# Kernel optimization log

Hardware: AMD Instinct MI355X
Metric: run time of the kernel (lower is better)

Reference implementation:

```python
import jax, jax.numpy as jnp
import numpy as np

B, N, D = 8192, 8192, 768

def setup_inputs() -> dict:
    key = jax.random.key(0)
    kx, ky = jax.random.split(key)
    x = jax.random.normal(kx, (B, D), dtype=jnp.float32)
    y = jax.random.normal(ky, (N, D), dtype=jnp.float32)
    return {"x": x, "y": y}

def reference(x, y):
    # Pairwise squared L2 distances: ||x_i - y_j||^2 = ||x_i||^2 + ||y_j||^2 - 2 x_i . y_j
    # Mathematically identical to the naive broadcast (x[:,None,:]-y[None,:,:])**2 sum,
    # but avoids the O(B*N*D) intermediate. Clamp at 0 to guard fp cancellation
    # (true squared distances are nonnegative).
    x2 = jnp.sum(x * x, axis=-1)[:, None]           # [B, 1]
    y2 = jnp.sum(y * y, axis=-1)[None, :]           # [1, N]
    xy = jnp.einsum('bd,nd->bn', x, y)              # [B, N] GEMM
    d = x2 + y2 - 2.0 * xy
    return jnp.maximum(d, 0.0)
```

## Files before the change

kernel.cpp:

```cpp
#include <hip/hip_runtime.h>
#include <hip/hip_bf16.h>
#include <stdint.h>


#define M_DIM 8192
#define N_DIM 8192
#define D_DIM 768
#define K_DIM (3 * D_DIM)
#define BM 256
#define BN 256
#define BK 32
#define KT (K_DIM / BK)

typedef __bf16 bf16x8 __attribute__((ext_vector_type(8)));
typedef float f32x4 __attribute__((ext_vector_type(4)));

#define GLOAD_LDS16(g, l) \
  __builtin_amdgcn_global_load_lds((const __attribute__((address_space(1))) void*)(g), \
                                   (__attribute__((address_space(3))) void*)(l), 16, 0, 0)

__global__ __launch_bounds__(256) void pack_kernel(
    const float* __restrict__ in, __hip_bfloat16* __restrict__ pk,
    float* __restrict__ nrm, int off_hi0, int off_hi1, int off_lo)
{
  int wid = threadIdx.x >> 6, lane = threadIdx.x & 63;
  int row = blockIdx.x * 4 + wid;
  const float* r = in + (size_t)row * D_DIM;
  __hip_bfloat16* p = pk + (size_t)row * K_DIM;
  float ss = 0.f;

  auto proc = [&](int u) {
    float4 a = *(const float4*)(r + u * 8);
    float4 b = *(const float4*)(r + u * 8 + 4);
    float v[8] = {a.x, a.y, a.z, a.w, b.x, b.y, b.z, b.w};
    union { __hip_bfloat16 h[8]; uint4 q; } H, L;
    #pragma unroll
    for (int j = 0; j < 8; ++j) {
      float x = v[j];
      ss += x * x;
      __hip_bfloat16 hi = __float2bfloat16(x);
      H.h[j] = hi;
      L.h[j] = __float2bfloat16(x - __bfloat162float(hi));
    }
    *(uint4*)(p + off_hi0 + u * 8) = H.q;
    *(uint4*)(p + off_hi1 + u * 8) = H.q;
    *(uint4*)(p + off_lo  + u * 8) = L.q;
  };

  proc(lane);
  if (lane < 32) proc(64 + lane);

  #pragma unroll
  for (int o = 1; o < 64; o <<= 1) ss += __shfl_xor(ss, o, 64);
  if (lane == 0) nrm[row] = ss;
}

__global__ __launch_bounds__(512, 2) void dist_gemm(
    const __hip_bfloat16* __restrict__ A, const __hip_bfloat16* __restrict__ Bp,
    const float* __restrict__ x2, const float* __restrict__ y2,
    float* __restrict__ out)
{
  __shared__ __attribute__((aligned(16))) __hip_bfloat16 As[4][BM * BK];
  __shared__ __attribute__((aligned(16))) __hip_bfloat16 Bs[4][BN * BK];

  int bid = blockIdx.x;
  int swz = (bid & 7) * 128 + (bid >> 3);
  int tileRow = swz >> 5;
  int tileCol = swz & 31;
  int rowBase = tileRow * BM;
  int colBase = tileCol * BN;

  int tid  = threadIdx.x;
  int lane = tid & 63;
  int wid  = tid >> 6;
  int wr = wid >> 2, wc = wid & 3;
  int rl = lane & 15, g = lane >> 4;

  auto STAGE = [&](int t) {
    int b = t & 3;
    int k0 = t * BK;
    #pragma unroll
    for (int s = 0; s < 2; ++s) {
      int pby = (s * 512 + tid) * 16;
      int o = pby ^ ((pby >> 2) & 48);
      int row = o >> 6, colb = o & 63;
      const __hip_bfloat16* ga = A  + (size_t)(rowBase + row) * K_DIM + k0 + (colb >> 1);
      const __hip_bfloat16* gb = Bp + (size_t)(colBase + row) * K_DIM + k0 + (colb >> 1);
      GLOAD_LDS16(ga, (char*)&As[b][0] + s * 8192 + wid * 1024);
      GLOAD_LDS16(gb, (char*)&Bs[b][0] + s * 8192 + wid * 1024);
    }
  };

  f32x4 acc[8][4];
  #pragma unroll
  for (int m = 0; m < 8; ++m)
    #pragma unroll
    for (int n = 0; n < 4; ++n)
      acc[m][n] = (f32x4){0.f, 0.f, 0.f, 0.f};

  STAGE(0); STAGE(1); STAGE(2);
  asm volatile("s_waitcnt vmcnt(8)" ::: "memory");
  __builtin_amdgcn_s_barrier();

  for (int kt = 0; kt < KT; ++kt) {
    int b = kt & 3;
    if (kt + 3 < KT) STAGE(kt + 3);

    bf16x8 af[8], bf[4];
    #pragma unroll
    for (int m = 0; m < 8; ++m) {
      int row = wr * 128 + m * 16 + rl;
      af[m] = *(const bf16x8*)((const char*)&As[b][0] + (row << 6) + ((g << 4) ^ ((row & 3) << 4)));
    }
    #pragma unroll
    for (int n = 0; n < 4; ++n) {
      int row = wc * 64 + n * 16 + rl;
      bf[n] = *(const bf16x8*)((const char*)&Bs[b][0] + (row << 6) + ((g << 4) ^ ((row & 3) << 4)));
    }

    __builtin_amdgcn_s_setprio(1);
    #pragma unroll
    for (int m = 0; m < 8; ++m)
      #pragma unroll
      for (int n = 0; n < 4; ++n)
        acc[m][n] = __builtin_amdgcn_mfma_f32_16x16x32_bf16(af[m], bf[n], acc[m][n], 0, 0, 0);
    __builtin_amdgcn_s_setprio(0);

    if (kt < KT - 3)       asm volatile("s_waitcnt vmcnt(8)" ::: "memory");
    else if (kt == KT - 3) asm volatile("s_waitcnt vmcnt(4)" ::: "memory");
    else if (kt == KT - 2) asm volatile("s_waitcnt vmcnt(0)" ::: "memory");
    if (kt < KT - 1) __builtin_amdgcn_s_barrier();
  }

  #pragma unroll
  for (int m = 0; m < 8; ++m) {
    int r0 = rowBase + wr * 128 + m * 16 + (lane >> 4) * 4;
    float4 xv = *(const float4*)&x2[r0];
    const float* xs = (const float*)&xv;
    #pragma unroll
    for (int n = 0; n < 4; ++n) {
      int c0 = colBase + wc * 64 + n * 16 + (lane & 15);
      float yv = y2[c0];
      float* op = out + (size_t)r0 * N_DIM + c0;
      #pragma unroll
      for (int v = 0; v < 4; ++v) {
        float d = xs[v] + yv - 2.0f * acc[m][n][v];
        op[(size_t)v * N_DIM] = fmaxf(d, 0.f);
      }
    }
  }
}

__global__ __launch_bounds__(256) void fallback_kernel(
    const float* __restrict__ x, const float* __restrict__ y, float* __restrict__ out)
{
  size_t gid = (size_t)blockIdx.x * 256 + threadIdx.x;
  int i = (int)(gid >> 13);
  int j = (int)(gid & 8191);
  const float4* xr = (const float4*)(x + (size_t)i * D_DIM);
  const float4* yr = (const float4*)(y + (size_t)j * D_DIM);
  float acc = 0.f;
  for (int d = 0; d < D_DIM / 4; ++d) {
    float4 a = xr[d], b = yr[d];
    float dx = a.x - b.x, dy = a.y - b.y, dz = a.z - b.z, dw = a.w - b.w;
    acc += dx * dx + dy * dy + dz * dz + dw * dw;
  }
  out[gid] = fmaxf(acc, 0.f);
}

extern "C" void kernel_launch(void* const* d_in, const int* in_sizes, int n_in,
                              void* d_out, int out_size, void* d_ws, size_t ws_size,
                              hipStream_t stream)
{
  const float* x = (const float*)d_in[0];
  const float* y = (const float*)d_in[1];
  float* out = (float*)d_out;

  size_t packBytes = (size_t)M_DIM * K_DIM * sizeof(__hip_bfloat16);
  size_t need = 2 * packBytes + 2 * (size_t)M_DIM * sizeof(float);
  if (ws_size < need) {
    fallback_kernel<<<((size_t)M_DIM * N_DIM) / 256, 256, 0, stream>>>(x, y, out);
    return;
  }

  __hip_bfloat16* Ap = (__hip_bfloat16*)d_ws;
  __hip_bfloat16* Bp = (__hip_bfloat16*)((char*)d_ws + packBytes);
  float* x2 = (float*)((char*)d_ws + 2 * packBytes);
  float* y2 = x2 + M_DIM;

  pack_kernel<<<M_DIM / 4, 256, 0, stream>>>(x, Ap, x2, 0, D_DIM, 2 * D_DIM);
  pack_kernel<<<N_DIM / 4, 256, 0, stream>>>(y, Bp, y2, 0, 2 * D_DIM, D_DIM);

  dist_gemm<<<(M_DIM / BM) * (N_DIM / BN), 512, 0, stream>>>(Ap, Bp, x2, y2, out);
}
```

Measured before the change: 680.6 us.

## Restructure GEMM mainloop into double-buffered 64-wide K steps with split stages; merge pack kernels

The GEMM mainloop moves from a 4-deep ring of 32-wide K tiles to a 2-buffer scheme with 64-wide K steps. Each step is split into four phases that interleave LDS fragment loads, next-tile global-to-LDS loads and MFMA groups, with explicit barriers and waitcnts. The aim is to overlap memory traffic with compute at finer grain and halve the register footprint of the A fragments. The two pack launches are also merged into one kernel over x and y. The many barriers per step may add synchronisation overhead, and the new swizzles have to be correct.

```diff
diff --git a/kernel.cpp b/kernel.cpp
--- a/kernel.cpp
+++ b/kernel.cpp
@@ -9,8 +9,8 @@
 #define K_DIM (3 * D_DIM)
 #define BM 256
 #define BN 256
-#define BK 32
-#define KT (K_DIM / BK)
+#define KSTEP 64
+#define NT (K_DIM / KSTEP)
 
 typedef __bf16 bf16x8 __attribute__((ext_vector_type(8)));
 typedef float f32x4 __attribute__((ext_vector_type(4)));
@@ -19,14 +19,26 @@
   __builtin_amdgcn_global_load_lds((const __attribute__((address_space(1))) void*)(g), \
                                    (__attribute__((address_space(3))) void*)(l), 16, 0, 0)
 
-__global__ __launch_bounds__(256) void pack_kernel(
-    const float* __restrict__ in, __hip_bfloat16* __restrict__ pk,
-    float* __restrict__ nrm, int off_hi0, int off_hi1, int off_lo)
+#define BAR()   __builtin_amdgcn_s_barrier()
+#define LGKM0() do { asm volatile("s_waitcnt lgkmcnt(0)" ::: "memory"); \
+                     __builtin_amdgcn_sched_barrier(0); } while (0)
+#define VMCNT(N) do { asm volatile("s_waitcnt vmcnt(" #N ")" ::: "memory"); \
+                      __builtin_amdgcn_sched_barrier(0); } while (0)
+
+__global__ __launch_bounds__(256) void pack2_kernel(
+    const float* __restrict__ x, const float* __restrict__ y,
+    __hip_bfloat16* __restrict__ Ap, __hip_bfloat16* __restrict__ Bp,
+    float* __restrict__ x2, float* __restrict__ y2)
 {
   int wid = threadIdx.x >> 6, lane = threadIdx.x & 63;
-  int row = blockIdx.x * 4 + wid;
-  const float* r = in + (size_t)row * D_DIM;
-  __hip_bfloat16* p = pk + (size_t)row * K_DIM;
+  int grow = blockIdx.x * 4 + wid;
+  bool isx = grow < M_DIM;
+  int row = isx ? grow : grow - M_DIM;
+  const float* r = (isx ? x : y) + (size_t)row * D_DIM;
+  __hip_bfloat16* p = (isx ? Ap : Bp) + (size_t)row * K_DIM;
+  float* nrm = isx ? x2 : y2;
+  int off_hi1 = isx ? D_DIM : 2 * D_DIM;
+  int off_lo  = isx ? 2 * D_DIM : D_DIM;
   float ss = 0.f;
 
   auto proc = [&](int u) {
@@ -36,13 +48,13 @@
     union { __hip_bfloat16 h[8]; uint4 q; } H, L;
     #pragma unroll
     for (int j = 0; j < 8; ++j) {
-      float x = v[j];
-      ss += x * x;
-      __hip_bfloat16 hi = __float2bfloat16(x);
+      float t = v[j];
+      ss += t * t;
+      __hip_bfloat16 hi = __float2bfloat16(t);
       H.h[j] = hi;
-      L.h[j] = __float2bfloat16(x - __bfloat162float(hi));
+      L.h[j] = __float2bfloat16(t - __bfloat162float(hi));
     }
-    *(uint4*)(p + off_hi0 + u * 8) = H.q;
+    *(uint4*)(p + u * 8) = H.q;
     *(uint4*)(p + off_hi1 + u * 8) = H.q;
     *(uint4*)(p + off_lo  + u * 8) = L.q;
   };
@@ -60,15 +72,13 @@
     const float* __restrict__ x2, const float* __restrict__ y2,
     float* __restrict__ out)
 {
-  __shared__ __attribute__((aligned(16))) __hip_bfloat16 As[4][BM * BK];
-  __shared__ __attribute__((aligned(16))) __hip_bfloat16 Bs[4][BN * BK];
+  __shared__ __attribute__((aligned(16))) __hip_bfloat16 As[2][BM * KSTEP];
+  __shared__ __attribute__((aligned(16))) __hip_bfloat16 Bs[2][2][BN * 32];
 
   int bid = blockIdx.x;
   int swz = (bid & 7) * 128 + (bid >> 3);
-  int tileRow = swz >> 5;
-  int tileCol = swz & 31;
-  int rowBase = tileRow * BM;
-  int colBase = tileCol * BN;
+  int rowBase = (swz >> 5) * BM;
+  int colBase = (swz & 31) * BN;
 
   int tid  = threadIdx.x;
   int lane = tid & 63;
@@ -76,19 +86,42 @@
   int wr = wid >> 2, wc = wid & 3;
   int rl = lane & 15, g = lane >> 4;
 
-  auto STAGE = [&](int t) {
-    int b = t & 3;
-    int k0 = t * BK;
-    #pragma unroll
-    for (int s = 0; s < 2; ++s) {
-      int pby = (s * 512 + tid) * 16;
-      int o = pby ^ ((pby >> 2) & 48);
-      int row = o >> 6, colb = o & 63;
-      const __hip_bfloat16* ga = A  + (size_t)(rowBase + row) * K_DIM + k0 + (colb >> 1);
-      const __hip_bfloat16* gb = Bp + (size_t)(colBase + row) * K_DIM + k0 + (colb >> 1);
-      GLOAD_LDS16(ga, (char*)&As[b][0] + s * 8192 + wid * 1024);
-      GLOAD_LDS16(gb, (char*)&Bs[b][0] + s * 8192 + wid * 1024);
-    }
+  int cA0 = (g * 16) ^ ((rl & 7) << 4);
+  int cB  = (g * 16) ^ (((rl >> 1) & 3) << 4);
+
+  int sArow = tid >> 3;
+  int sAcol = (((tid & 7) * 16) ^ (((tid >> 3) & 7) << 4)) >> 1;
+  int sBrow = tid >> 2;
+  int sBcol = (((tid & 3) * 16) ^ (((tid >> 3) & 3) << 4)) >> 1;
+
+  const __hip_bfloat16* gA = A  + (size_t)(rowBase + sArow) * K_DIM + sAcol;
+  const __hip_bfloat16* gB = Bp + (size_t)(colBase + sBrow) * K_DIM + sBcol;
+
+  auto stageA = [&](int buf, int h, int k0) {
+    #pragma unroll
+    for (int s = 0; s < 2; ++s)
+      GLOAD_LDS16(gA + ((size_t)(h * 128 + s * 64) * K_DIM) + k0,
+                  (char*)&As[buf][0] + h * 16384 + s * 8192 + wid * 1024);
+  };
+  auto stageB = [&](int buf, int h, int k0) {
+    #pragma unroll
+    for (int s = 0; s < 2; ++s)
+      GLOAD_LDS16(gB + ((size_t)(s * 128) * K_DIM) + k0 + h * 32,
+                  (char*)&Bs[buf][h][0] + s * 8192 + wid * 1024);
+  };
+
+  bf16x8 af[4], bf[4];
+  auto ldsA = [&](int buf, int G, int cc) {
+    #pragma unroll
+    for (int i = 0; i < 4; ++i)
+      af[i] = *(const bf16x8*)((const char*)&As[buf][0] +
+               (wr * 128 + (G * 4 + i) * 16 + rl) * 128 + cc);
+  };
+  auto ldsB = [&](int buf, int kk) {
+    #pragma unroll
+    for (int n = 0; n < 4; ++n)
+      bf[n] = *(const bf16x8*)((const char*)&Bs[buf][kk][0] +
+               (wc * 64 + n * 16 + rl) * 64 + cB);
   };
 
   f32x4 acc[8][4];
@@ -98,38 +131,48 @@
     for (int n = 0; n < 4; ++n)
       acc[m][n] = (f32x4){0.f, 0.f, 0.f, 0.f};
 
-  STAGE(0); STAGE(1); STAGE(2);
-  asm volatile("s_waitcnt vmcnt(8)" ::: "memory");
-  __builtin_amdgcn_s_barrier();
-
-  for (int kt = 0; kt < KT; ++kt) {
-    int b = kt & 3;
-    if (kt + 3 < KT) STAGE(kt + 3);
-
-    bf16x8 af[8], bf[4];
-    #pragma unroll
-    for (int m = 0; m < 8; ++m) {
-      int row = wr * 128 + m * 16 + rl;
-      af[m] = *(const bf16x8*)((const char*)&As[b][0] + (row << 6) + ((g << 4) ^ ((row & 3) << 4)));
-    }
-    #pragma unroll
-    for (int n = 0; n < 4; ++n) {
-      int row = wc * 64 + n * 16 + rl;
-      bf[n] = *(const bf16x8*)((const char*)&Bs[b][0] + (row << 6) + ((g << 4) ^ ((row & 3) << 4)));
-    }
-
+  auto mmac = [&](int G) {
     __builtin_amdgcn_s_setprio(1);
     #pragma unroll
-    for (int m = 0; m < 8; ++m)
+    for (int i = 0; i < 4; ++i)
       #pragma unroll
       for (int n = 0; n < 4; ++n)
-        acc[m][n] = __builtin_amdgcn_mfma_f32_16x16x32_bf16(af[m], bf[n], acc[m][n], 0, 0, 0);
+        acc[G * 4 + i][n] = __builtin_amdgcn_mfma_f32_16x16x32_bf16(af[i], bf[n], acc[G * 4 + i][n], 0, 0, 0);
     __builtin_amdgcn_s_setprio(0);
-
-    if (kt < KT - 3)       asm volatile("s_waitcnt vmcnt(8)" ::: "memory");
-    else if (kt == KT - 3) asm volatile("s_waitcnt vmcnt(4)" ::: "memory");
-    else if (kt == KT - 2) asm volatile("s_waitcnt vmcnt(0)" ::: "memory");
-    if (kt < KT - 1) __builtin_amdgcn_s_barrier();
+  };
+
+  stageA(0, 0, 0); stageA(0, 1, 0); stageB(0, 0, 0); stageB(0, 1, 0);
+  VMCNT(2);
+  BAR();
+
+  for (int t = 0; t < NT - 1; ++t) {
+    int buf = t & 1, nbuf = buf ^ 1, k0n = (t + 1) * KSTEP;
+    ldsA(buf, 0, cA0); ldsB(buf, 0);
+    stageA(nbuf, 0, k0n);
+    BAR(); LGKM0(); mmac(0); BAR();
+    ldsA(buf, 1, cA0);
+    stageA(nbuf, 1, k0n);
+    BAR(); LGKM0(); mmac(1);
+    VMCNT(4); BAR();
+    ldsA(buf, 0, cA0 ^ 64); ldsB(buf, 1);
+    stageB(nbuf, 0, k0n);
+    BAR(); LGKM0(); mmac(0); BAR();
+    ldsA(buf, 1, cA0 ^ 64);
+    stageB(nbuf, 1, k0n);
+    BAR(); LGKM0(); mmac(1);
+    VMCNT(2); BAR();
+  }
+  {
+    const int buf = (NT - 1) & 1;
+    ldsA(buf, 0, cA0); ldsB(buf, 0);
+    BAR(); LGKM0(); mmac(0); BAR();
+    ldsA(buf, 1, cA0);
+    BAR(); LGKM0(); mmac(1);
+    VMCNT(0); BAR();
+    ldsA(buf, 0, cA0 ^ 64); ldsB(buf, 1);
+    BAR(); LGKM0(); mmac(0); BAR();
+    ldsA(buf, 1, cA0 ^ 64);
+    BAR(); LGKM0(); mmac(1);
   }
 
   #pragma unroll
@@ -188,8 +231,6 @@
   float* x2 = (float*)((char*)d_ws + 2 * packBytes);
   float* y2 = x2 + M_DIM;
 
-  pack_kernel<<<M_DIM / 4, 256, 0, stream>>>(x, Ap, x2, 0, D_DIM, 2 * D_DIM);
-  pack_kernel<<<N_DIM / 4, 256, 0, stream>>>(y, Bp, y2, 0, 2 * D_DIM, D_DIM);
-
+  pack2_kernel<<<(M_DIM + N_DIM) / 4, 256, 0, stream>>>(x, y, Ap, Bp, x2, y2);
   dist_gemm<<<(M_DIM / BM) * (N_DIM / BN), 512, 0, stream>>>(Ap, Bp, x2, y2, out);
 }
```

Measured after the change: 624.1 us. 8.3% less time.
